# Kernel tuning notes

Measured on AMD Instinct MI355X. Metric: run time of the kernel, lower is better.

## Reference

```python
import jax, jax.numpy as jnp
import numpy as np
from jax import lax

# SLAYER neuron / simulation constants (from netParams yaml)
THETA = 1.0      # spike threshold
TS = 1.0         # simulation time step
TAU_SR = 10.0    # PSP (SRM) kernel time constant
TAU_REF = 1.0    # refractory kernel time constant
SCALE_REF = 2.0  # refractory kernel scale (x theta)
TAU_RHO = 1.0    # surrogate-gradient pdf width
SCALE_RHO = 1.0  # surrogate-gradient pdf scale
T_BINS = 2048    # nTimeBins = tSample / Ts
K_SRM = 100      # truncated SRM kernel length
K_REF = 32       # truncated refractory kernel length


def _srm_kernel():
    t = jnp.arange(K_SRM, dtype=jnp.float32) * TS
    return (t / TAU_SR) * jnp.exp(1.0 - t / TAU_SR)


def _ref_tail():
    # refractory response added to membrane at times t+1 .. t+K_REF after a spike
    t = jnp.arange(K_REF, dtype=jnp.float32) * TS
    ref = -SCALE_REF * THETA * (t / TAU_REF) * jnp.exp(1.0 - t / TAU_REF)
    return jnp.concatenate([ref[1:], jnp.zeros((1,), jnp.float32)])


SRM = _srm_kernel()
REF_TAIL = _ref_tail()


def psp(x):
    # causal temporal FIR along last axis: out[t] = sum_k SRM[k] * x[t-k]
    sh = x.shape
    xf = x.reshape(-1, 1, sh[-1])
    w = jnp.flip(SRM).reshape(1, 1, K_SRM).astype(x.dtype)
    y = lax.conv_general_dilated(xf, w, (1,), [(K_SRM - 1, 0)],
                                 dimension_numbers=('NCH', 'OIH', 'NCH'))
    return y.reshape(sh)


def _spike_scan(p):
    # p: [..., T]; sequential threshold + refractory dynamics over time
    pT = jnp.moveaxis(p, -1, 0)
    buf0 = jnp.zeros(p.shape[:-1] + (K_REF,), p.dtype)
    ref = REF_TAIL.astype(p.dtype)

    def step(buf, pt):
        u = pt + buf[..., 0]                      # membrane potential
        s = (u >= THETA).astype(p.dtype) / TS     # hard threshold spike
        buf = jnp.concatenate([buf[..., 1:], jnp.zeros_like(buf[..., :1])], -1) \
              + s[..., None] * ref
        return buf, (s, u)

    _, (sT, uT) = lax.scan(step, buf0, pT)
    return jnp.moveaxis(sT, 0, -1), jnp.moveaxis(uT, 0, -1)


@jax.custom_vjp
def spike(p):
    return _spike_scan(p)[0]


def _spike_fwd(p):
    s, u = _spike_scan(p)
    return s, u


def _spike_bwd(u, g):
    # SLAYER surrogate gradient: pdf of spike escape noise around threshold
    pdf = (SCALE_RHO / TAU_RHO) * jnp.exp(-jnp.abs(u - THETA) / TAU_RHO)
    return (g * pdf,)


spike.defvjp(_spike_fwd, _spike_bwd)


def conv2d_t(x, w):
    # x: [1,C,H,W,T]; same 2D 'VALID' conv applied at every time step
    xt = jnp.moveaxis(x[0], -1, 0)  # [T,C,H,W]
    y = lax.conv_general_dilated(xt, w, (1, 1), 'VALID',
                                 dimension_numbers=('NCHW', 'OIHW', 'NCHW'))
    return jnp.moveaxis(y, 0, -1)[None]


def pool_t(x):
    # SLAYER pool: per-channel 2x2 sum with constant weight 1.1*theta, stride 2
    _, C, H, W, T = x.shape
    xt = jnp.moveaxis(x[0], -1, 0).reshape(T * C, 1, H, W)
    w = jnp.full((1, 1, 2, 2), 1.1 * THETA, x.dtype)
    y = lax.conv_general_dilated(xt, w, (2, 2), 'VALID',
                                 dimension_numbers=('NCHW', 'OIHW', 'NCHW'))
    y = y.reshape(T, C, H // 2, W // 2)
    return jnp.moveaxis(y, 0, -1)[None]


def dense_t(x, w):
    # x: [1,Cin,1,1,T], w: [Cout,Cin] -> [1,Cout,1,1,T]
    return jnp.einsum('nchwt,oc->nohwt', x, w)


def forward(x, Wc1, Wc2, Wf1, Wf2, Wf3):
    # replicate(input, nTimeBins): nearest-interp == broadcast along new time axis
    xr = jnp.broadcast_to(x[..., None], x.shape + (T_BINS,)).reshape(1, 3, 32, 32, T_BINS)
    h = spike(psp(conv2d_t(xr, Wc1)))   # [1,6,28,28,T]
    h = spike(psp(pool_t(h)))           # [1,6,14,14,T]
    h = spike(psp(conv2d_t(h, Wc2)))    # [1,16,10,10,T]
    h = h.reshape(1, 16 * 10 * 10, 1, 1, T_BINS)
    h = spike(psp(dense_t(h, Wf1)))     # [1,300,1,1,T]
    h = spike(psp(dense_t(h, Wf2)))     # [1,150,1,1,T]
    h = spike(psp(dense_t(h, Wf3)))     # [1,10,1,1,T]
    return h


def setup_inputs() -> dict:
    key = jax.random.key(0)
    ks = jax.random.split(key, 6)
    x = jax.random.uniform(ks[0], (1, 3, 32, 32), jnp.float32)
    Wc1 = jax.random.normal(ks[1], (6, 3, 5, 5), jnp.float32) * 0.15
    Wc2 = jax.random.normal(ks[2], (16, 6, 5, 5), jnp.float32) * 0.08
    Wf1 = jax.random.normal(ks[3], (300, 1600), jnp.float32) * 0.03
    Wf2 = jax.random.normal(ks[4], (150, 300), jnp.float32) * 0.07
    Wf3 = jax.random.normal(ks[5], (10, 150), jnp.float32) * 0.1
    return {"x": x, "Wc1": Wc1, "Wc2": Wc2, "Wf1": Wf1, "Wf2": Wf2, "Wf3": Wf3}


def reference(x, Wc1, Wc2, Wf1, Wf2, Wf3):
    return forward(x, Wc1, Wc2, Wf1, Wf2, Wf3)
```

## Files before the change

kernel.cpp:

```cpp
#include <hip/hip_runtime.h>
#include <math.h>


#define T_BINS 2048
#define K_SRM  100
#define AEXP   0.36787944117144233
#define CHK    32
#define WUP    48
#define NCHK   (T_BINS / CHK)
#define FIXS   35184372088832.0
#define KSP    56

typedef __attribute__((ext_vector_type(8))) short          s16x8;
typedef __attribute__((ext_vector_type(8))) unsigned short u16x8;
typedef __attribute__((ext_vector_type(4))) float          f32x4;

__global__ __launch_bounds__(256) void k_prep(
    const float* __restrict__ x, const float* __restrict__ Wc1,
    const float* __restrict__ Wc2, const float* __restrict__ Wf1,
    const float* __restrict__ Wf2, const float* __restrict__ Wf3,
    float* __restrict__ c1, double* __restrict__ Scum, double* __restrict__ H,
    float* __restrict__ WT2, float* __restrict__ WT3,
    unsigned short* __restrict__ BL, unsigned short* __restrict__ BL2) {
  int b = blockIdx.x, tid = threadIdx.x;
  if (b < 19) {
    int idx = b * 256 + tid;
    if (idx >= 4704) return;
    int o = idx / 784, r = idx % 784, i = r / 28, j = r % 28;
    double acc = 0.0;
    for (int ci = 0; ci < 3; ++ci)
      for (int ky = 0; ky < 5; ++ky) {
        const float* xr = x + ci * 1024 + (i + ky) * 32 + j;
        const float* wr = Wc1 + ((o * 3 + ci) * 5 + ky) * 5;
#pragma unroll
        for (int kx = 0; kx < 5; ++kx)
          acc += (double)xr[kx] * (double)wr[kx];
      }
    c1[idx] = (float)acc;
  } else if (b < 299) {
    int idx = (b - 19) * 256 + tid;
    if (idx >= KSP * 320 * 4) return;
    int g = idx & 3, rest = idx >> 2;
    int n = rest % 320, ks = rest / 320;
    u16x8 out[6];
#pragma unroll
    for (int j = 0; j < 6; ++j)
#pragma unroll
      for (int jj = 0; jj < 8; ++jj) out[j][jj] = 0;
    if (n < 300 && ks < 50) {
      const float* wr = Wf1 + (size_t)n * 1600 + ks * 32 + g * 8;
#pragma unroll
      for (int jj = 0; jj < 8; ++jj) {
        long long v = llrint((double)wr[jj] * FIXS);
#pragma unroll
        for (int j = 0; j < 6; ++j) {
          int d = (int)(signed char)(v & 0xFF);
          v = (v - d) >> 8;
          float fd = (float)d;
          unsigned int fb = __float_as_uint(fd);
          out[j][jj] = (unsigned short)(fb >> 16);
        }
      }
    }
#pragma unroll
    for (int j = 0; j < 6; ++j)
      ((u16x8*)BL)[((j * KSP + ks) * 320 + n) * 4 + g] = out[j];
  } else if (b < 481) {
    int idx = (b - 299) * 256 + tid;
    if (idx < 45000) {
      int c = idx / 150, o = idx - c * 150;
      WT2[idx] = Wf2[o * 300 + c];
    } else if (idx < 46500) {
      int j = idx - 45000, c = j / 10, o = j - c * 10;
      WT3[j] = Wf3[o * 150 + c];
    }
  } else if (b < 483) {
    int idx = (b - 481) * 256 + tid;
    if (idx >= 320) return;
    int g = idx & 3, rest = idx >> 2;
    int o = rest & 15, ks = rest >> 4;
    u16x8 out[6];
#pragma unroll
    for (int j = 0; j < 6; ++j)
#pragma unroll
      for (int jj = 0; jj < 8; ++jj) out[j][jj] = 0;
#pragma unroll
    for (int jj = 0; jj < 8; ++jj) {
      int k = ks * 32 + g * 8 + jj;
      if (k < 150) {
        long long v = llrint((double)Wc2[o * 150 + k] * FIXS);
#pragma unroll
        for (int j = 0; j < 6; ++j) {
          int d = (int)(signed char)(v & 0xFF);
          v = (v - d) >> 8;
          float fd = (float)d;
          unsigned int fb = __float_as_uint(fd);
          out[j][jj] = (unsigned short)(fb >> 16);
        }
      }
    }
#pragma unroll
    for (int j = 0; j < 6; ++j)
      ((u16x8*)BL2)[((j * 5 + ks) * 4 + g) * 16 + o] = out[j];
  } else {
    if (tid == 0) {
      double acc = 0.0;
      for (int k = 0; k < K_SRM; ++k) {
        double tk = (double)k;
        double h = (tk * 0.1) * exp(1.0 - tk * 0.1);
        H[k] = h; acc += h; Scum[k] = acc;
      }
      H[100] = 0.0; H[101] = 0.0;
    }
  }
}

__global__ __launch_bounds__(256) void k_scan1_chunk(
    const float* __restrict__ c1, const double* __restrict__ Scum_g,
    unsigned char* __restrict__ s1b) {
  __shared__ double Sc[K_SRM];
  for (int k = threadIdx.x; k < K_SRM; k += 256) Sc[k] = Scum_g[k];
  __syncthreads();
  int idx = blockIdx.x * 256 + threadIdx.x;
  int chunk = idx / 4704, n = idx - chunk * 4704;
  int t0 = chunk * CHK;
  int ts = t0 - WUP; if (ts < 0) ts = 0;
  double w = (double)c1[n];
  double e1 = 0.0, e2 = 0.0;
  double u = w * Sc[ts < (K_SRM - 1) ? ts : (K_SRM - 1)];
  unsigned char* outp = s1b + n;
  for (int t = ts; t < t0; ++t) {
    double s = (u >= 1.0) ? 1.0 : 0.0;
    int si = t + 1 < (K_SRM - 1) ? t + 1 : (K_SRM - 1);
    u = w * Sc[si] - 2.0 * ((e1 + e2) + s);
    double t1 = e1 + s;
    e2 = AEXP * (e2 + t1); e1 = AEXP * t1;
  }
#pragma unroll 8
  for (int t = t0; t < t0 + CHK; ++t) {
    double s = (u >= 1.0) ? 1.0 : 0.0;
    outp[(size_t)t * 4704] = (unsigned char)s;
    int si = t + 1 < (K_SRM - 1) ? t + 1 : (K_SRM - 1);
    u = w * Sc[si] - 2.0 * ((e1 + e2) + s);
    double t1 = e1 + s;
    e2 = AEXP * (e2 + t1); e1 = AEXP * t1;
  }
}

__global__ __launch_bounds__(256) void k_pool(const unsigned char* __restrict__ s1b,
                                              unsigned char* __restrict__ y2b) {
  int idx = blockIdx.x * blockDim.x + threadIdx.x;
  if (idx >= 1176 * T_BINS) return;
  int t = idx / 1176, n2 = idx - t * 1176;
  int c = n2 / 196, r = n2 % 196, i = r / 14, j = r % 14;
  const unsigned char* b = s1b + (size_t)t * 4704 + c * 784 + (2 * i) * 28 + 2 * j;
  y2b[idx] = (unsigned char)((int)b[0] + (int)b[1] + (int)b[28] + (int)b[29]);
}

template <typename Tin, typename Tout>
__global__ __launch_bounds__(256) void k_psp_scan_chunk(
    const Tin* __restrict__ z, Tout* __restrict__ sout, int N,
    long strideT, long strideN, const double* __restrict__ H_g,
    double A1, double A2, double B1, double C0, double C1, double xscale) {
  __shared__ double Hs[102];
  for (int k = threadIdx.x; k < 102; k += 256) Hs[k] = H_g[k];
  __syncthreads();
  int idx = blockIdx.x * blockDim.x + threadIdx.x;
  if (idx >= NCHK * N) return;
  int chunk = idx / N, n = idx - chunk * N;
  int t0 = chunk * CHK;
  int ts = t0 - WUP; if (ts < 0) ts = 0;
  const Tin* zn = z + n;

  double accA = 0.0, accB = 0.0;
  float fA[10], fB[10];
#define LOADF(BUF, J0)                                               \
  { _Pragma("unroll")                                                \
    for (int q_ = 0; q_ < 10; ++q_)                                  \
      BUF[q_] = (float)zn[(long)(ts - 1 - ((J0) + q_)) * (long)N]; }
#define FMA10(BUF, J0)                                               \
  { _Pragma("unroll")                                                \
    for (int q_ = 0; q_ < 10; ++q_) {                                \
      double v_ = (double)BUF[q_];                                   \
      accA += Hs[(J0) + q_ + 1] * v_;                                \
      accB += Hs[(J0) + q_] * v_;                                    \
    } }
  LOADF(fA, 0)
  for (int q = 0; q < 100; q += 20) {
    LOADF(fB, q + 10)
    FMA10(fA, q)
    LOADF(fA, q + 20)
    FMA10(fB, q + 10)
  }
#undef LOADF
#undef FMA10
  double pp1 = accA * xscale;
  double pp2 = accB * xscale;
  double xm100 = (double)(float)zn[(long)(ts - 100) * (long)N];
  double u = pp1, e1 = 0.0, e2 = 0.0;

  float cA[8], cB[8], lA[8], lB[8];
  size_t oa = (size_t)n * (size_t)strideN + (size_t)t0 * (size_t)strideT;
  int nwg = (t0 - ts) >> 3;
  int ngrp = nwg + CHK / 8;
#define PREF8(CBUF, LBUF, TB)                                        \
  { long tb_ = (long)(TB);                                           \
    _Pragma("unroll")                                                \
    for (int j_ = 0; j_ < 8; ++j_) {                                 \
      CBUF[j_] = (float)zn[(tb_ + j_) * (long)N];                    \
      LBUF[j_] = (float)zn[(tb_ + j_ - 99) * (long)N];               \
    } }
#define PROC8(CBUF, LBUF, DOSTORE)                                   \
  { _Pragma("unroll")                                                \
    for (int j_ = 0; j_ < 8; ++j_) {                                 \
      double s = (u >= 1.0) ? 1.0 : 0.0;                             \
      if (DOSTORE) { sout[oa] = (Tout)s; oa += (size_t)strideT; }    \
      double xt = (double)CBUF[j_], x99 = (double)LBUF[j_];          \
      double pn = A1 * pp1 - A2 * pp2 + B1 * xt - C0 * x99           \
                  + C1 * xm100;                                      \
      xm100 = x99;                                                   \
      u = pn - 2.0 * ((e1 + e2) + s);                                \
      double t1 = e1 + s;                                            \
      e2 = AEXP * (e2 + t1); e1 = AEXP * t1;                         \
      pp2 = pp1; pp1 = pn;                                           \
    } }
  PREF8(cA, lA, ts)
  for (int g = 0; g < ngrp; g += 2) {
    PREF8(cB, lB, ts + (g + 1) * 8)
    PROC8(cA, lA, g >= nwg)
    PREF8(cA, lA, ts + (g + 2) * 8)
    PROC8(cB, lB, g + 1 >= nwg)
  }
#undef PREF8
#undef PROC8
}

__global__ __launch_bounds__(256, 2) void k_conv2_mfma(
    const unsigned char* __restrict__ s2b, const unsigned short* __restrict__ BL2g,
    float* __restrict__ z3) {
  __shared__ __align__(16) unsigned short bl2[15360];
  __shared__ unsigned char ls[4][1216];
  __shared__ int tab[160];
  int tid = threadIdx.x;
  for (int i = tid; i < 7680; i += 256)
    ((unsigned int*)bl2)[i] = ((const unsigned int*)BL2g)[i];
  if (tid < 160) {
    int k = tid;
    int ci = k / 25, rem = k - ci * 25;
    int ky = rem / 5, kx = rem - ky * 5;
    tab[k] = (k < 150) ? (ci * 196 + ky * 14 + kx) : 0;
  }
  int w = tid >> 6, lane = tid & 63;
  int t = blockIdx.x * 4 + w;
  {
    const unsigned int* srow = (const unsigned int*)(s2b + (size_t)t * 1176);
    unsigned int* dst = (unsigned int*)ls[w];
    for (int i = lane; i < 294; i += 64) dst[i] = srow[i];
  }
  __syncthreads();
  int r = lane & 15, g = lane >> 4;
#pragma unroll
  for (int mt = 0; mt < 7; ++mt) {
    int p = mt * 16 + r;
    int pi = p / 10;
    int pioff = pi * 14 + (p - pi * 10);
    s16x8 a[5];
#pragma unroll
    for (int ks = 0; ks < 5; ++ks) {
      u16x8 f;
#pragma unroll
      for (int jj = 0; jj < 8; ++jj) {
        int k = ks * 32 + g * 8 + jj;
        bool v = (mt < 6 || p < 100) && (ks < 4 || k < 150);
        int idx = v ? (tab[k] + pioff) : 0;
        unsigned char byte = ls[w][idx];
        f[jj] = (v && byte) ? (unsigned short)0x3F80 : (unsigned short)0;
      }
      a[ks] = (s16x8)f;
    }
    double zacc[4] = {0.0, 0.0, 0.0, 0.0};
    double scale = 1.0;
    for (int j = 0; j < 6; ++j) {
      f32x4 C = (f32x4){0.f, 0.f, 0.f, 0.f};
#pragma unroll
      for (int ks = 0; ks < 5; ++ks) {
        const u16x8* bf = (const u16x8*)bl2 + (((j * 5 + ks) * 4 + g) * 16 + r);
        C = __builtin_amdgcn_mfma_f32_16x16x32_bf16(a[ks], (s16x8)(*bf), C, 0, 0, 0);
      }
#pragma unroll
      for (int q = 0; q < 4; ++q) zacc[q] += scale * (double)C[q];
      scale *= 256.0;
    }
#pragma unroll
    for (int q = 0; q < 4; ++q) {
      int pr = mt * 16 + g * 4 + q;
      if (pr < 100)
        z3[(size_t)t * 1600 + r * 100 + pr] = (float)(zacc[q] * (1.0 / FIXS));
    }
  }
}

__global__ __launch_bounds__(512, 2) void k_mfma_dense1(
    const unsigned char* __restrict__ s3b, const unsigned short* __restrict__ BL,
    float* __restrict__ z4) {
  __shared__ float redf[8][64][41];
  int bid = blockIdx.x;
  int xcd = bid & 7;
  int ct = xcd & 3;
  int bm = (bid >> 3) | ((xcd >> 2) << 5);
  int col0 = ct * 80;
  int w = threadIdx.x >> 6, lane = threadIdx.x & 63;
  int r = lane & 15, g = lane >> 4;
  int ks0 = w * 7;
  int rowA = bm * 32 + r, rowB = rowA + 16;
  const unsigned char* abA = s3b + (size_t)rowA * 1600 + ks0 * 32 + g * 8;
  const unsigned char* abB = s3b + (size_t)rowB * 1600 + ks0 * 32 + g * 8;

  s16x8 aA[7], aB[7];
#pragma unroll
  for (int ks = 0; ks < 7; ++ks) {
    unsigned long long bA = *(const unsigned long long*)(abA + ks * 32);
    unsigned long long bB = *(const unsigned long long*)(abB + ks * 32);
    u16x8 fa, fb;
#pragma unroll
    for (int jj = 0; jj < 8; ++jj) {
      fa[jj] = ((bA >> (8 * jj)) & 1ULL) ? (unsigned short)0x3F80
                                         : (unsigned short)0;
      fb[jj] = ((bB >> (8 * jj)) & 1ULL) ? (unsigned short)0x3F80
                                         : (unsigned short)0;
    }
    aA[ks] = (s16x8)fa; aB[ks] = (s16x8)fb;
  }

  double zawA[4] = {0.0, 0.0, 0.0, 0.0};
  double zawB[4] = {0.0, 0.0, 0.0, 0.0};
  double scale = 1.0;
  for (int j = 0; j < 6; ++j) {
    f32x4 CA[5], CB[5];
#pragma unroll
    for (int nt = 0; nt < 5; ++nt) {
      CA[nt] = (f32x4){0.f, 0.f, 0.f, 0.f};
      CB[nt] = (f32x4){0.f, 0.f, 0.f, 0.f};
    }
#pragma unroll
    for (int ks = 0; ks < 7; ++ks) {
      const u16x8* bb =
          (const u16x8*)BL + ((size_t)((j * KSP + ks0 + ks) * 320 + col0 + r)) * 4 + g;
#pragma unroll
      for (int nt = 0; nt < 5; ++nt) {
        s16x8 bf = (s16x8)bb[nt * 64];
        CA[nt] = __builtin_amdgcn_mfma_f32_16x16x32_bf16(aA[ks], bf, CA[nt], 0, 0, 0);
        CB[nt] = __builtin_amdgcn_mfma_f32_16x16x32_bf16(aB[ks], bf, CB[nt], 0, 0, 0);
      }
    }
#pragma unroll
    for (int nt = 0; nt < 5; ++nt)
#pragma unroll
      for (int q = 0; q < 4; ++q) {
        redf[w][lane][nt * 4 + q]      = CA[nt][q];
        redf[w][lane][20 + nt * 4 + q] = CB[nt][q];
      }
    __syncthreads();
    if (w < 5) {
#pragma unroll
      for (int q = 0; q < 4; ++q) {
        int i = w * 4 + q;
        float sA = ((redf[0][lane][i] + redf[1][lane][i]) +
                    (redf[2][lane][i] + redf[3][lane][i])) +
                   ((redf[4][lane][i] + redf[5][lane][i]) +
                    (redf[6][lane][i] + redf[7][lane][i]));
        int i2 = 20 + i;
        float sB = ((redf[0][lane][i2] + redf[1][lane][i2]) +
                    (redf[2][lane][i2] + redf[3][lane][i2])) +
                   ((redf[4][lane][i2] + redf[5][lane][i2]) +
                    (redf[6][lane][i2] + redf[7][lane][i2]));
        zawA[q] += scale * (double)sA;
        zawB[q] += scale * (double)sB;
      }
    }
    __syncthreads();
    scale *= 256.0;
  }

  if (w < 5) {
    int col = col0 + w * 16 + r;
    if (col < 300) {
      int rA0 = bm * 32 + g * 4, rB0 = rA0 + 16;
#pragma unroll
      for (int q = 0; q < 4; ++q) {
        z4[(size_t)(rA0 + q) * 300 + col] = (float)(zawA[q] * (1.0 / FIXS));
        z4[(size_t)(rB0 + q) * 300 + col] = (float)(zawB[q] * (1.0 / FIXS));
      }
    }
  }
}

template <int NIN, int NOUT, int BLK>
__global__ __launch_bounds__(BLK) void k_dense_sparse(
    const unsigned char* __restrict__ s, const float* __restrict__ WT,
    float* __restrict__ z) {
  constexpr int NCH = (NIN + BLK - 1) / BLK;
  constexpr int NW = BLK / 64;
  __shared__ __align__(16) int list[NIN];
  __shared__ int wcnt[NCH][NW];
  int t = blockIdx.x;
  const unsigned char* srow = s + (size_t)t * NIN;
  int tid = threadIdx.x, lane = tid & 63, wv = tid >> 6;
  unsigned long long msave[NCH];
  bool asave[NCH];
#pragma unroll
  for (int ci = 0; ci < NCH; ++ci) {
    int c = ci * BLK + tid;
    bool a = (c < NIN) && (srow[c] != 0);
    unsigned long long m = __ballot(a);
    msave[ci] = m; asave[ci] = a;
    if (lane == 0) wcnt[ci][wv] = __popcll(m);
  }
  __syncthreads();
  int nact = 0;
#pragma unroll
  for (int ci = 0; ci < NCH; ++ci) {
    int off = nact;
    for (int w = 0; w < wv; ++w) off += wcnt[ci][w];
    if (asave[ci])
      list[off + __popcll(msave[ci] & ((1ULL << lane) - 1))] = ci * BLK + tid;
    for (int w = 0; w < NW; ++w) nact += wcnt[ci][w];
  }
  __syncthreads();
  if (tid >= NOUT) return;
  const float* col = WT + tid;
  double a0 = 0.0, a1 = 0.0, a2 = 0.0, a3 = 0.0;
  int k = 0, nact4 = nact & ~3;
  for (; k < nact4; k += 4) {
    int4 l4 = *(const int4*)&list[k];
    a0 += (double)col[(size_t)l4.x * NOUT];
    a1 += (double)col[(size_t)l4.y * NOUT];
    a2 += (double)col[(size_t)l4.z * NOUT];
    a3 += (double)col[(size_t)l4.w * NOUT];
  }
  for (; k < nact; ++k) a0 += (double)col[(size_t)list[k] * NOUT];
  z[(size_t)t * NOUT + tid] = (float)((a0 + a1) + (a2 + a3));
}

extern "C" void kernel_launch(void* const* d_in, const int* in_sizes, int n_in,
                              void* d_out, int out_size, void* d_ws, size_t ws_size,
                              hipStream_t stream) {
  const float* x   = (const float*)d_in[0];
  const float* Wc1 = (const float*)d_in[1];
  const float* Wc2 = (const float*)d_in[2];
  const float* Wf1 = (const float*)d_in[3];
  const float* Wf2 = (const float*)d_in[4];
  const float* Wf3 = (const float*)d_in[5];
  float* out = (float*)d_out;
  char* ws = (char*)d_ws;

  double* Scum = (double*)(ws + 0);
  double* Htab = (double*)(ws + 2048);
  float*  c1   = (float*)(ws + 4096);
  const size_t PADZ = 65536;
  const size_t ZA   = PADZ + 655360;
  const size_t PADY = ZA + 13107200 + 262144;
  const size_t Y2B  = PADY + 131072;
  const size_t S1B  = Y2B + 2408448 + 65536;
  const size_t S2B  = S1B + 9633792;
  const size_t S3B  = S2B + 2408448;
  const size_t S4B  = S3B + 3276800;
  const size_t S5B  = S4B + 614400;
  const size_t WB   = S5B + 307200;
  const size_t WC   = WB + 180000;
  const size_t BLa  = 33122000;
  const size_t BL2a = BLa + 6881280;
  float* zA = (float*)(ws + ZA);
  unsigned char* y2b = (unsigned char*)(ws + Y2B);
  unsigned char* s1b = (unsigned char*)(ws + S1B);
  unsigned char* s2b = (unsigned char*)(ws + S2B);
  unsigned char* s3b = (unsigned char*)(ws + S3B);
  unsigned char* s4b = (unsigned char*)(ws + S4B);
  unsigned char* s5b = (unsigned char*)(ws + S5B);
  float* WT2 = (float*)(ws + WB);
  float* WT3 = (float*)(ws + WC);
  unsigned short* BLp  = (unsigned short*)(ws + BLa);
  unsigned short* BL2p = (unsigned short*)(ws + BL2a);

  double b = exp(-0.1), c = 0.1 * exp(1.0);
  double A1 = 2.0 * b, A2 = b * b;
  double B1 = c * b;
  double C0 = 100.0 * c * pow(b, 100.0);
  double C1 = 99.0 * c * pow(b, 101.0);
  double sc = (double)1.1f;

  hipMemsetAsync(ws + PADZ, 0, 655360, stream);
  hipMemsetAsync(ws + PADY, 0, 131072, stream);
  k_prep<<<484, 256, 0, stream>>>(x, Wc1, Wc2, Wf1, Wf2, Wf3, c1, Scum, Htab,
                                  WT2, WT3, BLp, BL2p);
  k_scan1_chunk<<<NCHK * 4704 / 256, 256, 0, stream>>>(c1, Scum, s1b);
  k_pool<<<(1176 * T_BINS) / 256, 256, 0, stream>>>(s1b, y2b);
  k_psp_scan_chunk<unsigned char, unsigned char>
      <<<(NCHK * 1176 + 255) / 256, 256, 0, stream>>>(
      y2b, s2b, 1176, 1176L, 1L, Htab, A1, A2, B1 * sc, C0 * sc, C1 * sc, sc);
  k_conv2_mfma<<<T_BINS / 4, 256, 0, stream>>>(s2b, BL2p, zA);
  k_psp_scan_chunk<float, unsigned char>
      <<<(NCHK * 1600 + 255) / 256, 256, 0, stream>>>(
      zA, s3b, 1600, 1600L, 1L, Htab, A1, A2, B1, C0, C1, 1.0);
  k_mfma_dense1<<<256, 512, 0, stream>>>(s3b, BLp, zA);
  k_psp_scan_chunk<float, unsigned char>
      <<<(NCHK * 300 + 255) / 256, 256, 0, stream>>>(
      zA, s4b, 300, 300L, 1L, Htab, A1, A2, B1, C0, C1, 1.0);
  k_dense_sparse<300, 150, 192><<<T_BINS, 192, 0, stream>>>(s4b, WT2, zA);
  k_psp_scan_chunk<float, unsigned char>
      <<<(NCHK * 150 + 255) / 256, 256, 0, stream>>>(
      zA, s5b, 150, 150L, 1L, Htab, A1, A2, B1, C0, C1, 1.0);
  k_dense_sparse<150, 10, 64><<<T_BINS, 64, 0, stream>>>(s5b, WT3, zA);
  k_psp_scan_chunk<float, float>
      <<<(NCHK * 10 + 255) / 256, 256, 0, stream>>>(
      zA, out, 10, 1L, 2048L, Htab, A1, A2, B1, C0, C1, 1.0);

  (void)in_sizes; (void)n_in; (void)out_size; (void)ws_size;
}
```

Measured before the change: 198.8 us.

## Split dense1 MFMA reduction across two K-chunk blocks with combine kernel

The dense1 MFMA kernel now splits the 1600-wide reduction into two K halves handled by separate blocks, doubling the grid to 512 blocks. Each wave computes a single 16-row tile, which halves accumulator registers and shrinks the LDS reduction buffer so the launch bound allows four blocks per CU. Partial fixed-point sums are written as doubles to a scratch area and a new combine kernel adds the two halves and rescales to float. The aim is more parallelism and occupancy, paid for by an extra launch and extra global traffic for the double-precision partials.

```diff
diff --git a/kernel.cpp b/kernel.cpp
--- a/kernel.cpp
+++ b/kernel.cpp
@@ -300,99 +300,108 @@
   }
 }
 
-__global__ __launch_bounds__(512, 2) void k_mfma_dense1(
+__global__ __launch_bounds__(512, 4) void k_mfma_dense1(
     const unsigned char* __restrict__ s3b, const unsigned short* __restrict__ BL,
-    float* __restrict__ z4) {
-  __shared__ float redf[8][64][41];
+    double* __restrict__ zpart) {
+  __shared__ float redf[8][64][21];
   int bid = blockIdx.x;
   int xcd = bid & 7;
   int ct = xcd & 3;
-  int bm = (bid >> 3) | ((xcd >> 2) << 5);
+  int kc = xcd >> 2;
+  int bm = bid >> 3;
   int col0 = ct * 80;
   int w = threadIdx.x >> 6, lane = threadIdx.x & 63;
   int r = lane & 15, g = lane >> 4;
-  int ks0 = w * 7;
-  int rowA = bm * 32 + r, rowB = rowA + 16;
-  const unsigned char* abA = s3b + (size_t)rowA * 1600 + ks0 * 32 + g * 8;
-  const unsigned char* abB = s3b + (size_t)rowB * 1600 + ks0 * 32 + g * 8;
-
-  s16x8 aA[7], aB[7];
+  int sub = w >> 2, kch = w & 3;
+  int ks0 = kc * 28 + kch * 7;
+  int row = bm * 32 + sub * 16 + r;
+  const unsigned char* ab = s3b + (size_t)row * 1600 + ks0 * 32 + g * 8;
+
+  s16x8 a[7];
 #pragma unroll
   for (int ks = 0; ks < 7; ++ks) {
-    unsigned long long bA = *(const unsigned long long*)(abA + ks * 32);
-    unsigned long long bB = *(const unsigned long long*)(abB + ks * 32);
-    u16x8 fa, fb;
-#pragma unroll
-    for (int jj = 0; jj < 8; ++jj) {
-      fa[jj] = ((bA >> (8 * jj)) & 1ULL) ? (unsigned short)0x3F80
-                                         : (unsigned short)0;
-      fb[jj] = ((bB >> (8 * jj)) & 1ULL) ? (unsigned short)0x3F80
-                                         : (unsigned short)0;
-    }
-    aA[ks] = (s16x8)fa; aB[ks] = (s16x8)fb;
-  }
-
-  double zawA[4] = {0.0, 0.0, 0.0, 0.0};
-  double zawB[4] = {0.0, 0.0, 0.0, 0.0};
+    unsigned long long bits = *(const unsigned long long*)(ab + ks * 32);
+    u16x8 f;
+#pragma unroll
+    for (int jj = 0; jj < 8; ++jj)
+      f[jj] = ((bits >> (8 * jj)) & 1ULL) ? (unsigned short)0x3F80
+                                          : (unsigned short)0;
+    a[ks] = (s16x8)f;
+  }
+
+  double zawP[4] = {0.0, 0.0, 0.0, 0.0};
+  double zawS[4] = {0.0, 0.0, 0.0, 0.0};
   double scale = 1.0;
   for (int j = 0; j < 6; ++j) {
-    f32x4 CA[5], CB[5];
-#pragma unroll
-    for (int nt = 0; nt < 5; ++nt) {
-      CA[nt] = (f32x4){0.f, 0.f, 0.f, 0.f};
-      CB[nt] = (f32x4){0.f, 0.f, 0.f, 0.f};
-    }
+    f32x4 C[5];
+#pragma unroll
+    for (int nt = 0; nt < 5; ++nt) C[nt] = (f32x4){0.f, 0.f, 0.f, 0.f};
 #pragma unroll
     for (int ks = 0; ks < 7; ++ks) {
       const u16x8* bb =
           (const u16x8*)BL + ((size_t)((j * KSP + ks0 + ks) * 320 + col0 + r)) * 4 + g;
 #pragma unroll
-      for (int nt = 0; nt < 5; ++nt) {
-        s16x8 bf = (s16x8)bb[nt * 64];
-        CA[nt] = __builtin_amdgcn_mfma_f32_16x16x32_bf16(aA[ks], bf, CA[nt], 0, 0, 0);
-        CB[nt] = __builtin_amdgcn_mfma_f32_16x16x32_bf16(aB[ks], bf, CB[nt], 0, 0, 0);
-      }
+      for (int nt = 0; nt < 5; ++nt)
+        C[nt] = __builtin_amdgcn_mfma_f32_16x16x32_bf16(
+            a[ks], (s16x8)bb[nt * 64], C[nt], 0, 0, 0);
     }
 #pragma unroll
     for (int nt = 0; nt < 5; ++nt)
 #pragma unroll
+      for (int q = 0; q < 4; ++q)
+        redf[w][lane][nt * 4 + q] = C[nt][q];
+    __syncthreads();
+    {
+      int s = w / 5, nt = w - s * 5;
+      int base = s * 4;
+#pragma unroll
       for (int q = 0; q < 4; ++q) {
-        redf[w][lane][nt * 4 + q]      = CA[nt][q];
-        redf[w][lane][20 + nt * 4 + q] = CB[nt][q];
-      }
-    __syncthreads();
-    if (w < 5) {
+        int i = nt * 4 + q;
+        float sm = (redf[base + 0][lane][i] + redf[base + 1][lane][i]) +
+                   (redf[base + 2][lane][i] + redf[base + 3][lane][i]);
+        zawP[q] += scale * (double)sm;
+      }
+    }
+    if (w < 2) {
+      int nt = 3 + w;
 #pragma unroll
       for (int q = 0; q < 4; ++q) {
-        int i = w * 4 + q;
-        float sA = ((redf[0][lane][i] + redf[1][lane][i]) +
-                    (redf[2][lane][i] + redf[3][lane][i])) +
-                   ((redf[4][lane][i] + redf[5][lane][i]) +
-                    (redf[6][lane][i] + redf[7][lane][i]));
-        int i2 = 20 + i;
-        float sB = ((redf[0][lane][i2] + redf[1][lane][i2]) +
-                    (redf[2][lane][i2] + redf[3][lane][i2])) +
-                   ((redf[4][lane][i2] + redf[5][lane][i2]) +
-                    (redf[6][lane][i2] + redf[7][lane][i2]));
-        zawA[q] += scale * (double)sA;
-        zawB[q] += scale * (double)sB;
+        int i = nt * 4 + q;
+        float sm = (redf[4][lane][i] + redf[5][lane][i]) +
+                   (redf[6][lane][i] + redf[7][lane][i]);
+        zawS[q] += scale * (double)sm;
       }
     }
     __syncthreads();
     scale *= 256.0;
   }
 
-  if (w < 5) {
-    int col = col0 + w * 16 + r;
-    if (col < 300) {
-      int rA0 = bm * 32 + g * 4, rB0 = rA0 + 16;
-#pragma unroll
-      for (int q = 0; q < 4; ++q) {
-        z4[(size_t)(rA0 + q) * 300 + col] = (float)(zawA[q] * (1.0 / FIXS));
-        z4[(size_t)(rB0 + q) * 300 + col] = (float)(zawB[q] * (1.0 / FIXS));
-      }
-    }
-  }
+  double* zp = zpart + (size_t)kc * (2048 * 320);
+  {
+    int s = w / 5, nt = w - s * 5;
+    int rowo = bm * 32 + s * 16 + g * 4;
+    int col = col0 + nt * 16 + r;
+#pragma unroll
+    for (int q = 0; q < 4; ++q)
+      zp[(size_t)(rowo + q) * 320 + col] = zawP[q];
+  }
+  if (w < 2) {
+    int nt = 3 + w;
+    int rowo = bm * 32 + 16 + g * 4;
+    int col = col0 + nt * 16 + r;
+#pragma unroll
+    for (int q = 0; q < 4; ++q)
+      zp[(size_t)(rowo + q) * 320 + col] = zawS[q];
+  }
+}
+
+__global__ __launch_bounds__(256) void k_combine1(const double* __restrict__ zpart,
+                                                  float* __restrict__ z4) {
+  int idx = blockIdx.x * 256 + threadIdx.x;
+  if (idx >= 2048 * 300) return;
+  int t = idx / 300, o = idx - t * 300;
+  size_t b = (size_t)t * 320 + o;
+  z4[idx] = (float)((zpart[b] + zpart[b + 655360]) * (1.0 / FIXS));
 }
 
 template <int NIN, int NOUT, int BLK>
@@ -481,6 +490,7 @@
   float* WT3 = (float*)(ws + WC);
   unsigned short* BLp  = (unsigned short*)(ws + BLa);
   unsigned short* BL2p = (unsigned short*)(ws + BL2a);
+  double* zpart = (double*)(ws + PADY);
 
   double b = exp(-0.1), c = 0.1 * exp(1.0);
   double A1 = 2.0 * b, A2 = b * b;
@@ -502,7 +512,8 @@
   k_psp_scan_chunk<float, unsigned char>
       <<<(NCHK * 1600 + 255) / 256, 256, 0, stream>>>(
       zA, s3b, 1600, 1600L, 1L, Htab, A1, A2, B1, C0, C1, 1.0);
-  k_mfma_dense1<<<256, 512, 0, stream>>>(s3b, BLp, zA);
+  k_mfma_dense1<<<512, 512, 0, stream>>>(s3b, BLp, zpart);
+  k_combine1<<<(2048 * 300 + 255) / 256, 256, 0, stream>>>(zpart, zA);
   k_psp_scan_chunk<float, unsigned char>
       <<<(NCHK * 300 + 255) / 256, 256, 0, stream>>>(
       zA, s4b, 300, 300L, 1L, Htab, A1, A2, B1, C0, C1, 1.0);
```

New measurement: 212.3 us. 1.07x slower.
